# Kernel optimization log

Hardware: AMD Instinct MI355X
Metric: run time of the kernel (lower is better)

## Reference

```python
import jax, jax.numpy as jnp
import numpy as np

B, H, W, C = 2, 96, 192, 768
NH, HD = 12, 64
W0, W1 = 8, 8          # window size
S0, S1 = 4, 4          # shift size
N = W0 * W1
NW = (H // W0) * (W // W1)
HID = 3072             # mlp_ratio 4 * dim
SCALE = HD ** -0.5


def _ln(x, g, b):
    m = x.mean(-1, keepdims=True)
    v = ((x - m) ** 2).mean(-1, keepdims=True)
    return (x - m) * jax.lax.rsqrt(v + 1e-5) * g + b


def _partition(x):  # (B,H,W,C) -> (B*NW, W0, W1, C)
    Bb = x.shape[0]
    x = x.reshape(Bb, H // W0, W0, W // W1, W1, -1).transpose(0, 1, 3, 2, 4, 5)
    return x.reshape(-1, W0, W1, x.shape[-1])


def _reverse(w):  # (B*NW, W0, W1, C) -> (B,H,W,C)
    Cc = w.shape[-1]
    x = w.reshape(B, H // W0, W // W1, W0, W1, Cc).transpose(0, 1, 3, 2, 4, 5)
    return x.reshape(B, H, W, Cc)


def _rope2(x):  # axial 2D RoPE on (nB, W0, W1, HD): first half rotates over h, second over w
    dh = HD // 2

    def cs(L, d):
        inv = 1.0 / (10000.0 ** (jnp.arange(0, d, 2, dtype=jnp.float32) / d))
        ang = jnp.arange(L, dtype=jnp.float32)[:, None] * inv
        return jnp.cos(ang), jnp.sin(ang)

    def rot(xa, cos, sin):
        x1, x2 = xa[..., 0::2], xa[..., 1::2]
        return jnp.stack([x1 * cos - x2 * sin, x1 * sin + x2 * cos], -1).reshape(xa.shape)

    ch, sh = cs(W0, dh)
    cw, sw = cs(W1, dh)
    xh = rot(x[..., :dh], ch[:, None, :], sh[:, None, :])
    xw = rot(x[..., dh:], cw[None, :, :], sw[None, :, :])
    return jnp.concatenate([xh, xw], -1)


def _make_mask():
    # faithful port of BasicLayer.create_mask (2D path)
    img = np.zeros((H, W), np.float32)
    cnt = 0
    for hs in (slice(0, -W0), slice(-W0, -S0), slice(-S0, None)):
        for wsl in (slice(0, -W1), slice(-W1, 0), slice(0, None)):
            img[hs, wsl] = cnt
            cnt += 1
    mw = img.reshape(H // W0, W0, W // W1, W1).transpose(0, 2, 1, 3).reshape(NW, N)
    am = mw[:, None, :] - mw[:, :, None]
    return jnp.asarray(np.where(am != 0, -100.0, 0.0).astype(np.float32))


def setup_inputs():
    key = jax.random.key(0)
    ks = jax.random.split(key, 6)
    s = lambda k, shape, fan: jax.random.normal(k, shape, jnp.float32) * (fan ** -0.5)
    return dict(
        x=jax.random.normal(ks[0], (B, H * W, C), jnp.float32),
        mask=_make_mask(),
        w_qkv=s(ks[1], (3 * C, C), C), b_qkv=jnp.zeros((3 * C,), jnp.float32),
        w_proj=s(ks[2], (C, C), C), b_proj=jnp.zeros((C,), jnp.float32),
        g1=jnp.ones((C,), jnp.float32), b1=jnp.zeros((C,), jnp.float32),
        g2=jnp.ones((C,), jnp.float32), b2=jnp.zeros((C,), jnp.float32),
        w_fc1=s(ks[3], (HID, C), C), b_fc1=jnp.zeros((HID,), jnp.float32),
        w_fc2=s(ks[4], (C, HID), HID), b_fc2=jnp.zeros((C,), jnp.float32),
    )


def reference(x, mask, w_qkv, b_qkv, w_proj, b_proj, g1, b1, g2, b2,
              w_fc1, b_fc1, w_fc2, b_fc2):
    shortcut = x
    xi = x.reshape(B, H, W, C)
    xi = jnp.roll(xi, (-S0, -S1), axis=(1, 2))
    xw = _partition(xi).reshape(-1, N, C)  # (B*NW, N, C)
    B_ = xw.shape[0]
    qkv = (xw @ w_qkv.T + b_qkv).reshape(B_, N, 3, NH, HD).transpose(2, 0, 3, 1, 4)
    q, k, v = qkv[0], qkv[1], qkv[2]  # (B_, NH, N, HD)
    q = _rope2(q.reshape(-1, W0, W1, HD)).reshape(B_, NH, N, HD)
    k = _rope2(k.reshape(-1, W0, W1, HD)).reshape(B_, NH, N, HD)
    attn = jnp.einsum('bhnd,bhmd->bhnm', q * SCALE, k)
    attn = attn.reshape(B, NW, NH, N, N) + mask[None, :, None]
    attn = jax.nn.softmax(attn.reshape(B_, NH, N, N), axis=-1)
    out = jnp.einsum('bhnm,bhmd->bnhd', attn, v).reshape(B_, N, C)
    out = out @ w_proj.T + b_proj
    xr = _reverse(out.reshape(-1, W0, W1, C))
    xr = jnp.roll(xr, (S0, S1), axis=(1, 2)).reshape(B, H * W, C)
    x1 = _ln(shortcut + xr, g1, b1)          # post-norm residual, as in source
    h = jax.nn.relu(x1 @ w_fc1.T + b_fc1) @ w_fc2.T + b_fc2
    return _ln(x1 + h, g2, b2)
```

## Files before the change

### kernel.cpp

```cpp
#include <hip/hip_runtime.h>
#include <math.h>
#include <stddef.h>

#define NTOK   36864
#define CDIM   768
#define HIDDIM 3072
#define QKVDIM 2304

typedef unsigned short u16;
typedef unsigned int   u32;
typedef __attribute__((ext_vector_type(8))) short short8;
typedef __attribute__((ext_vector_type(4))) float f32x4;

__device__ __forceinline__ float bf2f(u16 h) { return __uint_as_float(((u32)h) << 16); }
__device__ __forceinline__ u16 f2bf(float f) {
  u32 u = __float_as_uint(f);
  u32 r = u + 0x7fffu + ((u >> 16) & 1u);
  return (u16)(r >> 16);
}

__device__ __forceinline__ int win_row_to_src(int r) {
  int n = r & 63;
  int wflat = r >> 6;
  int b = wflat / 288;
  int wi = wflat - b * 288;
  int wh = wi / 24;
  int ww = wi - wh * 24;
  int i0 = n >> 3, i1 = n & 7;
  int hh = wh * 8 + i0 + 4; if (hh >= 96)  hh -= 96;
  int wp = ww * 8 + i1 + 4; if (wp >= 192) wp -= 192;
  return b * 18432 + hh * 192 + wp;
}

__device__ __forceinline__ void load_lds16(const u16* g, u16* l) {
  __builtin_amdgcn_global_load_lds((const __attribute__((address_space(1))) void*)g,
                                   (__attribute__((address_space(3))) void*)l, 16, 0, 0);
}

template<int OUTBF, int RELU, int RES>
__launch_bounds__(512, 2)
__global__ void gemm256(const u16* __restrict__ A, const u16* __restrict__ Wt,
                        const float* __restrict__ bias, const u16* __restrict__ res,
                        void* __restrict__ Cout, int M, int N, int K,
                        int gridx, int nwg)
{
  const int orig = blockIdx.x;
  const int xcd  = orig & 7;
  const int q    = nwg >> 3, r8 = nwg & 7;
  const int wgid = (xcd < r8 ? xcd * (q + 1) : r8 * (q + 1) + (xcd - r8) * q) + (orig >> 3);
  const int bn   = (wgid % gridx) * 256;
  const int bm   = (wgid / gridx) * 256;

  __shared__ __align__(16) u16 lds[2][2][256 * 64];

  const int t    = threadIdx.x;
  const int wv   = t >> 6, lane = t & 63;
  const int wm   = wv >> 2, wn = wv & 3;
  const int lr   = lane & 15, lg = lane >> 4;
  const int sr   = t >> 3;
  const int ss   = t & 7;

  const u16* Abase = A  + (size_t)bm * K;
  const u16* Bbase = Wt + (size_t)bn * K;

  const int nt = K >> 6;

  auto stage = [&](int kt, int b) {
    const int k0 = kt << 6;
#pragma unroll
    for (int j = 0; j < 4; j++) {
      int row  = j * 64 + sr;
      int slot = ss ^ (row & 7);
      load_lds16(Abase + (size_t)row * K + k0 + slot * 8, &lds[b][0][j * 4096 + t * 8]);
    }
#pragma unroll
    for (int j = 0; j < 4; j++) {
      int row  = j * 64 + sr;
      int slot = ss ^ (row & 7);
      load_lds16(Bbase + (size_t)row * K + k0 + slot * 8, &lds[b][1][j * 4096 + t * 8]);
    }
  };

  f32x4 acc[8][4] = {};

  stage(0, 0);
  stage(1, 1);

  for (int tt = 0; tt < nt; tt++) {
    const int cur = tt & 1;
    if (tt + 1 < nt) asm volatile("s_waitcnt vmcnt(8)" ::: "memory");
    else             asm volatile("s_waitcnt vmcnt(0)" ::: "memory");
    __builtin_amdgcn_s_barrier();

    const u16* Ab = &lds[cur][0][0];
    const u16* Bb = &lds[cur][1][0];

    short8 bfr[4][2], afr[4][2];
#pragma unroll
    for (int nf = 0; nf < 4; nf++)
#pragma unroll
      for (int ks = 0; ks < 2; ks++) {
        int row = wn * 64 + nf * 16 + lr;
        bfr[nf][ks] = *(const short8*)(Bb + row * 64 + (((ks * 4 + lg) ^ (row & 7)) << 3));
      }
#pragma unroll
    for (int mf = 0; mf < 4; mf++)
#pragma unroll
      for (int ks = 0; ks < 2; ks++) {
        int row = wm * 128 + mf * 16 + lr;
        afr[mf][ks] = *(const short8*)(Ab + row * 64 + (((ks * 4 + lg) ^ (row & 7)) << 3));
      }
    asm volatile("s_waitcnt lgkmcnt(0)" ::: "memory");
    __builtin_amdgcn_sched_barrier(0);
    __builtin_amdgcn_s_setprio(1);
#pragma unroll
    for (int ks = 0; ks < 2; ks++)
#pragma unroll
      for (int mf = 0; mf < 4; mf++)
#pragma unroll
        for (int nf = 0; nf < 4; nf++)
          acc[mf][nf] = __builtin_amdgcn_mfma_f32_16x16x32_bf16(afr[mf][ks], bfr[nf][ks], acc[mf][nf], 0, 0, 0);
    __builtin_amdgcn_s_setprio(0);

    short8 afr2[4][2];
#pragma unroll
    for (int mf = 0; mf < 4; mf++)
#pragma unroll
      for (int ks = 0; ks < 2; ks++) {
        int row = wm * 128 + (mf + 4) * 16 + lr;
        afr2[mf][ks] = *(const short8*)(Ab + row * 64 + (((ks * 4 + lg) ^ (row & 7)) << 3));
      }
    asm volatile("s_waitcnt lgkmcnt(0)" ::: "memory");
    __builtin_amdgcn_sched_barrier(0);
    __builtin_amdgcn_s_barrier();

    if (tt + 2 < nt) stage(tt + 2, cur);

    __builtin_amdgcn_s_setprio(1);
#pragma unroll
    for (int ks = 0; ks < 2; ks++)
#pragma unroll
      for (int mf = 0; mf < 4; mf++)
#pragma unroll
        for (int nf = 0; nf < 4; nf++)
          acc[mf + 4][nf] = __builtin_amdgcn_mfma_f32_16x16x32_bf16(afr2[mf][ks], bfr[nf][ks], acc[mf + 4][nf], 0, 0, 0);
    __builtin_amdgcn_s_setprio(0);
  }

#pragma unroll
  for (int nf = 0; nf < 4; nf++) {
    int col = bn + wn * 64 + nf * 16 + lr;
    float bcol = bias[col];
#pragma unroll
    for (int mf = 0; mf < 8; mf++) {
#pragma unroll
      for (int j = 0; j < 4; j++) {
        int row = bm + wm * 128 + mf * 16 + lg * 4 + j;
        float v = acc[mf][nf][j] + bcol;
        if (RELU) v = fmaxf(v, 0.f);
        if (RES)  v += bf2f(res[(size_t)row * N + col]);
        if (OUTBF) ((u16*)Cout)[(size_t)row * N + col] = f2bf(v);
        else       ((float*)Cout)[(size_t)row * N + col] = v;
      }
    }
  }
}

__launch_bounds__(256)
__global__ void gather_x_bf16(const float* __restrict__ x, u16* __restrict__ xg)
{
  const int r = blockIdx.x, t = threadIdx.x;
  const float* src = x + (size_t)win_row_to_src(r) * CDIM;
  u16* dst = xg + (size_t)r * CDIM;
#pragma unroll
  for (int e = 0; e < 3; e++) dst[t + 256 * e] = f2bf(src[t + 256 * e]);
}

__launch_bounds__(256)
__global__ void conv_bf16(const float* __restrict__ in, u16* __restrict__ out, int n)
{
  int i = blockIdx.x * 256 + threadIdx.x;
  if (i < n) out[i] = f2bf(in[i]);
}

__launch_bounds__(256)
__global__ void attn_mfma(const u16* __restrict__ qkv, const float* __restrict__ mask,
                          u16* __restrict__ out, int bw0)
{
  __shared__ u16 vt[4][4096];
  __shared__ u16 pbuf[4][4096];
  __shared__ float ropetab[512];

  const int t = threadIdx.x;
  {
    int p = t >> 3, pos = t & 7;
    float inv = __expf(-(float)(p & 15) * 0.5756462732485115f);
    float sv, cv;
    sincosf((float)pos * inv, &sv, &cv);
    ropetab[t * 2]     = cv;
    ropetab[t * 2 + 1] = sv;
  }
  __syncthreads();

  const int wv = t >> 6, lane = t & 63;
  const int lr = lane & 15, lg = lane >> 4;
  const int gp   = blockIdx.x * 4 + wv;
  const int head = gp % 12;
  const int lw   = gp / 12;
  const int bwg  = bw0 + lw;
  const int widx = bwg % 288;
  const u16* base = qkv + (size_t)lw * 64 * QKVDIM + head * 64;

  {
    const u16* vrow = base + 1536 + (size_t)lane * QKVDIM;
    u16* vb = vt[wv];
#pragma unroll
    for (int s = 0; s < 8; s++) {
      short8 v = *(const short8*)(vrow + s * 8);
#pragma unroll
      for (int j = 0; j < 8; j++) {
        int d = s * 8 + j;
        vb[d * 64 + ((((lane >> 3) ^ (d & 7)) << 3) | (lane & 7))] = (u16)v[j];
      }
    }
  }

  short8 aq[4][2], ak[4][2];
#pragma unroll
  for (int f = 0; f < 4; f++) {
#pragma unroll
    for (int ks = 0; ks < 2; ks++) {
      int n = f * 16 + lr;
      short8 qv = *(const short8*)(base + (size_t)n * QKVDIM + ks * 32 + lg * 8);
      short8 kv = *(const short8*)(base + (size_t)n * QKVDIM + 768 + ks * 32 + lg * 8);
      short8 qo, ko;
#pragma unroll
      for (int jj = 0; jj < 4; jj++) {
        int p   = ks * 16 + lg * 4 + jj;
        int pos = (p < 16) ? (n >> 3) : (n & 7);
        float cv = ropetab[(p * 8 + pos) * 2];
        float sv = ropetab[(p * 8 + pos) * 2 + 1];
        float q1 = bf2f((u16)qv[2 * jj]), q2 = bf2f((u16)qv[2 * jj + 1]);
        float k1 = bf2f((u16)kv[2 * jj]), k2 = bf2f((u16)kv[2 * jj + 1]);
        qo[2 * jj]     = (short)f2bf((q1 * cv - q2 * sv) * 0.125f);
        qo[2 * jj + 1] = (short)f2bf((q1 * sv + q2 * cv) * 0.125f);
        ko[2 * jj]     = (short)f2bf(k1 * cv - k2 * sv);
        ko[2 * jj + 1] = (short)f2bf(k1 * sv + k2 * cv);
      }
      aq[f][ks] = qo; ak[f][ks] = ko;
    }
  }

  f32x4 sf[4][4] = {};
#pragma unroll
  for (int ks = 0; ks < 2; ks++)
#pragma unroll
    for (int fn = 0; fn < 4; fn++)
#pragma unroll
      for (int fm = 0; fm < 4; fm++)
        sf[fn][fm] = __builtin_amdgcn_mfma_f32_16x16x32_bf16(aq[fn][ks], ak[fm][ks], sf[fn][fm], 0, 0, 0);

  const float* mrow = mask + (size_t)widx * 4096;
#pragma unroll
  for (int fn = 0; fn < 4; fn++)
#pragma unroll
    for (int fm = 0; fm < 4; fm++)
#pragma unroll
      for (int j = 0; j < 4; j++)
        sf[fn][fm][j] += mrow[(fn * 16 + lg * 4 + j) * 64 + fm * 16 + lr];

#pragma unroll
  for (int fn = 0; fn < 4; fn++) {
#pragma unroll
    for (int j = 0; j < 4; j++) {
      float m0 = fmaxf(fmaxf(sf[fn][0][j], sf[fn][1][j]),
                       fmaxf(sf[fn][2][j], sf[fn][3][j]));
      m0 = fmaxf(m0, __shfl_xor(m0, 1));
      m0 = fmaxf(m0, __shfl_xor(m0, 2));
      m0 = fmaxf(m0, __shfl_xor(m0, 4));
      m0 = fmaxf(m0, __shfl_xor(m0, 8));
      float s0 = 0.f;
#pragma unroll
      for (int fm = 0; fm < 4; fm++) {
        float e = __expf(sf[fn][fm][j] - m0);
        sf[fn][fm][j] = e;
        s0 += e;
      }
      s0 += __shfl_xor(s0, 1);
      s0 += __shfl_xor(s0, 2);
      s0 += __shfl_xor(s0, 4);
      s0 += __shfl_xor(s0, 8);
      float r = 1.f / s0;
#pragma unroll
      for (int fm = 0; fm < 4; fm++) sf[fn][fm][j] *= r;
    }
  }

  u16* pb = pbuf[wv];
#pragma unroll
  for (int fn = 0; fn < 4; fn++)
#pragma unroll
    for (int fm = 0; fm < 4; fm++)
#pragma unroll
      for (int j = 0; j < 4; j++) {
        int n = fn * 16 + lg * 4 + j, m = fm * 16 + lr;
        pb[n * 64 + ((((m >> 3) ^ (n & 7)) << 3) | (m & 7))] = f2bf(sf[fn][fm][j]);
      }
  asm volatile("s_waitcnt lgkmcnt(0)" ::: "memory");
  __builtin_amdgcn_sched_barrier(0);

  short8 ap[4][2], bvf[4][2];
#pragma unroll
  for (int f = 0; f < 4; f++)
#pragma unroll
    for (int ks = 0; ks < 2; ks++) {
      int rn = f * 16 + lr;
      ap[f][ks]  = *(const short8*)(pb     + rn * 64 + (((ks * 4 + lg) ^ (rn & 7)) << 3));
      bvf[f][ks] = *(const short8*)(vt[wv] + rn * 64 + (((ks * 4 + lg) ^ (rn & 7)) << 3));
    }
  f32x4 o[4][4] = {};
#pragma unroll
  for (int ks = 0; ks < 2; ks++)
#pragma unroll
    for (int fn = 0; fn < 4; fn++)
#pragma unroll
      for (int fd = 0; fd < 4; fd++)
        o[fn][fd] = __builtin_amdgcn_mfma_f32_16x16x32_bf16(ap[fn][ks], bvf[fd][ks], o[fn][fd], 0, 0, 0);

  u16* ob = out + ((size_t)bwg * 64) * CDIM + head * 64;
#pragma unroll
  for (int fn = 0; fn < 4; fn++)
#pragma unroll
    for (int fd = 0; fd < 4; fd++)
#pragma unroll
      for (int j = 0; j < 4; j++) {
        int n = fn * 16 + lg * 4 + j, d = fd * 16 + lr;
        ob[(size_t)n * CDIM + d] = f2bf(o[fn][fd][j]);
      }
}

__launch_bounds__(256)
__global__ void ln1_kernel(const float* __restrict__ xin, const u16* __restrict__ add,
                           const float* __restrict__ g, const float* __restrict__ bb,
                           u16* __restrict__ out)
{
  const int tok = blockIdx.x;
  int b = tok / 18432;
  int hw = tok - b * 18432;
  int h = hw / 192, w = hw - h * 192;
  int h2 = h - 4; if (h2 < 0) h2 += 96;
  int w2 = w - 4; if (w2 < 0) w2 += 192;
  int r = ((b * 12 + (h2 >> 3)) * 24 + (w2 >> 3)) * 64 + (h2 & 7) * 8 + (w2 & 7);
  const float* a0 = xin + (size_t)tok * CDIM;
  const u16*   a1 = add + (size_t)r * CDIM;

  const int t = threadIdx.x;
  float v[3];
  float s1 = 0.f, s2 = 0.f;
#pragma unroll
  for (int e = 0; e < 3; e++) {
    float x = a0[t + 256 * e] + bf2f(a1[t + 256 * e]);
    v[e] = x; s1 += x; s2 += x * x;
  }
  __shared__ float r1[256], r2[256];
  r1[t] = s1; r2[t] = s2;
  __syncthreads();
  for (int o = 128; o > 0; o >>= 1) {
    if (t < o) { r1[t] += r1[t + o]; r2[t] += r2[t + o]; }
    __syncthreads();
  }
  float mean = r1[0] * (1.f / 768.f);
  float var  = r2[0] * (1.f / 768.f) - mean * mean;
  float rs   = rsqrtf(var + 1e-5f);
#pragma unroll
  for (int e = 0; e < 3; e++) {
    int c = t + 256 * e;
    out[(size_t)tok * CDIM + c] = f2bf((v[e] - mean) * rs * g[c] + bb[c]);
  }
}

__launch_bounds__(256)
__global__ void ln2_kernel(const u16* __restrict__ xin, const float* __restrict__ g,
                           const float* __restrict__ bb, float* __restrict__ out)
{
  const int tok = blockIdx.x;
  const u16* a0 = xin + (size_t)tok * CDIM;
  const int t = threadIdx.x;
  float v[3];
  float s1 = 0.f, s2 = 0.f;
#pragma unroll
  for (int e = 0; e < 3; e++) {
    float x = bf2f(a0[t + 256 * e]);
    v[e] = x; s1 += x; s2 += x * x;
  }
  __shared__ float r1[256], r2[256];
  r1[t] = s1; r2[t] = s2;
  __syncthreads();
  for (int o = 128; o > 0; o >>= 1) {
    if (t < o) { r1[t] += r1[t + o]; r2[t] += r2[t + o]; }
    __syncthreads();
  }
  float mean = r1[0] * (1.f / 768.f);
  float var  = r2[0] * (1.f / 768.f) - mean * mean;
  float rs   = rsqrtf(var + 1e-5f);
#pragma unroll
  for (int e = 0; e < 3; e++) {
    int c = t + 256 * e;
    out[(size_t)tok * CDIM + c] = (v[e] - mean) * rs * g[c] + bb[c];
  }
}

static inline void launch_gemm(const u16* A, const u16* Wt, const float* bias,
                               const u16* res, void* C, int M, int N, int K,
                               int outbf, int relu, int resf, hipStream_t s)
{
  int gridx = N / 256, nwg = gridx * (M / 256);
  if (outbf) {
    if (relu)      gemm256<1,1,0><<<nwg, 512, 0, s>>>(A, Wt, bias, res, C, M, N, K, gridx, nwg);
    else if (resf) gemm256<1,0,1><<<nwg, 512, 0, s>>>(A, Wt, bias, res, C, M, N, K, gridx, nwg);
    else           gemm256<1,0,0><<<nwg, 512, 0, s>>>(A, Wt, bias, res, C, M, N, K, gridx, nwg);
  } else {
    gemm256<0,0,0><<<nwg, 512, 0, s>>>(A, Wt, bias, res, C, M, N, K, gridx, nwg);
  }
}

extern "C" void kernel_launch(void* const* d_in, const int* in_sizes, int n_in,
                              void* d_out, int out_size, void* d_ws, size_t ws_size,
                              hipStream_t stream)
{
  const float* x      = (const float*)d_in[0];
  const float* mask   = (const float*)d_in[1];
  const float* w_qkv  = (const float*)d_in[2];
  const float* b_qkv  = (const float*)d_in[3];
  const float* w_proj = (const float*)d_in[4];
  const float* b_proj = (const float*)d_in[5];
  const float* g1     = (const float*)d_in[6];
  const float* b1     = (const float*)d_in[7];
  const float* g2     = (const float*)d_in[8];
  const float* b2     = (const float*)d_in[9];
  const float* w_fc1  = (const float*)d_in[10];
  const float* b_fc1  = (const float*)d_in[11];
  const float* w_fc2  = (const float*)d_in[12];
  const float* b_fc2  = (const float*)d_in[13];
  float* out = (float*)d_out;

  char* base = (char*)d_ws;
  u16* R1 = (u16*)base;
  u16* R2 = (u16*)(base + 56623104);
  u16* AO = R2 + 28311552;
  u16* R3 = (u16*)(base + 56623104 + 113246208);
  u16* wqkvb  = (u16*)(base + 56623104 + 113246208 + 56623104);
  u16* wprojb = wqkvb  + 1769472;
  u16* wfc1b  = wprojb + 589824;
  u16* wfc2b  = wfc1b  + 2359296;

  conv_bf16<<<(1769472 + 255) / 256, 256, 0, stream>>>(w_qkv,  wqkvb,  1769472);
  conv_bf16<<<( 589824 + 255) / 256, 256, 0, stream>>>(w_proj, wprojb,  589824);
  conv_bf16<<<(2359296 + 255) / 256, 256, 0, stream>>>(w_fc1,  wfc1b,  2359296);
  conv_bf16<<<(2359296 + 255) / 256, 256, 0, stream>>>(w_fc2,  wfc2b,  2359296);
  gather_x_bf16<<<NTOK, 256, 0, stream>>>(x, R1);

  for (int c = 0; c < 3; c++) {
    launch_gemm(R1 + (size_t)c * 12288 * CDIM, wqkvb, b_qkv, nullptr, R2,
                12288, QKVDIM, CDIM, 1, 0, 0, stream);
    attn_mfma<<<576, 256, 0, stream>>>(R2, mask, AO, c * 192);
  }

  launch_gemm(AO, wprojb, b_proj, nullptr, R3, NTOK, CDIM, CDIM, 1, 0, 0, stream);

  ln1_kernel<<<NTOK, 256, 0, stream>>>(x, R3, g1, b1, R1);

  for (int c = 0; c < 2; c++) {
    const u16* x1c = R1 + (size_t)c * 18432 * CDIM;
    launch_gemm(x1c, wfc1b, b_fc1, nullptr, R2, 18432, HIDDIM, CDIM, 1, 1, 0, stream);
    launch_gemm(R2, wfc2b, b_fc2, x1c, R3 + (size_t)c * 18432 * CDIM,
                18432, CDIM, HIDDIM, 1, 0, 1, stream);
  }

  ln2_kernel<<<NTOK, 256, 0, stream>>>(R3, g2, b2, out);
}
```

Measured before the change: 953.8 us.

## Restructure GEMM main loop into 8-phase half-tile ping-pong pipeline

```diff
diff --git a/kernel.cpp b/kernel.cpp
--- a/kernel.cpp
+++ b/kernel.cpp
@@ -37,6 +37,11 @@
                                    (__attribute__((address_space(3))) void*)l, 16, 0, 0);
 }
 
+#define GBAR()  __builtin_amdgcn_s_barrier()
+#define LGKM0() do { asm volatile("s_waitcnt lgkmcnt(0)" ::: "memory"); \
+                     __builtin_amdgcn_sched_barrier(0); } while (0)
+#define VMC4()  asm volatile("s_waitcnt vmcnt(4)" ::: "memory")
+
 template<int OUTBF, int RELU, int RES>
 __launch_bounds__(512, 2)
 __global__ void gemm256(const u16* __restrict__ A, const u16* __restrict__ Wt,
@@ -57,106 +62,118 @@
   const int wv   = t >> 6, lane = t & 63;
   const int wm   = wv >> 2, wn = wv & 3;
   const int lr   = lane & 15, lg = lane >> 4;
-  const int sr   = t >> 3;
-  const int ss   = t & 7;
+  const int rl   = t >> 3;
+  const int sc   = t & 7;
 
   const u16* Abase = A  + (size_t)bm * K;
   const u16* Bbase = Wt + (size_t)bn * K;
 
-  const int nt = K >> 6;
-
-  auto stage = [&](int kt, int b) {
+  const int nt   = K >> 6;
+  const int half = nt >> 1;
+
+  auto stageA = [&](int kt, int mh, int b) {
     const int k0 = kt << 6;
 #pragma unroll
-    for (int j = 0; j < 4; j++) {
-      int row  = j * 64 + sr;
-      int slot = ss ^ (row & 7);
-      load_lds16(Abase + (size_t)row * K + k0 + slot * 8, &lds[b][0][j * 4096 + t * 8]);
-    }
-#pragma unroll
-    for (int j = 0; j < 4; j++) {
-      int row  = j * 64 + sr;
-      int slot = ss ^ (row & 7);
-      load_lds16(Bbase + (size_t)row * K + k0 + slot * 8, &lds[b][1][j * 4096 + t * 8]);
+    for (int j = 0; j < 2; j++) {
+      int row  = j * 128 + mh * 64 + rl;
+      int slot = sc ^ (row & 7);
+      load_lds16(Abase + (size_t)row * K + k0 + slot * 8, &lds[b][0][row * 64 + sc * 8]);
     }
   };
+  auto stageB = [&](int kt, int nh, int b) {
+    const int k0 = kt << 6;
+#pragma unroll
+    for (int j = 0; j < 2; j++) {
+      int row  = j * 128 + nh * 32 + rl + (rl & 32);
+      int slot = sc ^ (row & 7);
+      load_lds16(Bbase + (size_t)row * K + k0 + slot * 8, &lds[b][1][row * 64 + sc * 8]);
+    }
+  };
+
+  short8 af[4][2], bf0[2][2], bf1[2][2];
+  auto lda = [&](const u16* Ab, int mh) {
+#pragma unroll
+    for (int mf = 0; mf < 4; mf++)
+#pragma unroll
+      for (int ks = 0; ks < 2; ks++) {
+        int row = wm * 128 + mh * 64 + mf * 16 + lr;
+        af[mf][ks] = *(const short8*)(Ab + row * 64 + (((ks * 4 + lg) ^ (row & 7)) << 3));
+      }
+  };
+  auto ldb = [&](const u16* Bb, int nh, short8 bf[2][2]) {
+#pragma unroll
+    for (int nf = 0; nf < 2; nf++)
+#pragma unroll
+      for (int ks = 0; ks < 2; ks++) {
+        int row = wn * 64 + nh * 32 + nf * 16 + lr;
+        bf[nf][ks] = *(const short8*)(Bb + row * 64 + (((ks * 4 + lg) ^ (row & 7)) << 3));
+      }
+  };
 
   f32x4 acc[8][4] = {};
-
-  stage(0, 0);
-  stage(1, 1);
-
-  for (int tt = 0; tt < nt; tt++) {
-    const int cur = tt & 1;
-    if (tt + 1 < nt) asm volatile("s_waitcnt vmcnt(8)" ::: "memory");
-    else             asm volatile("s_waitcnt vmcnt(0)" ::: "memory");
-    __builtin_amdgcn_s_barrier();
-
-    const u16* Ab = &lds[cur][0][0];
-    const u16* Bb = &lds[cur][1][0];
-
-    short8 bfr[4][2], afr[4][2];
-#pragma unroll
-    for (int nf = 0; nf < 4; nf++)
-#pragma unroll
-      for (int ks = 0; ks < 2; ks++) {
-        int row = wn * 64 + nf * 16 + lr;
-        bfr[nf][ks] = *(const short8*)(Bb + row * 64 + (((ks * 4 + lg) ^ (row & 7)) << 3));
-      }
-#pragma unroll
-    for (int mf = 0; mf < 4; mf++)
-#pragma unroll
-      for (int ks = 0; ks < 2; ks++) {
-        int row = wm * 128 + mf * 16 + lr;
-        afr[mf][ks] = *(const short8*)(Ab + row * 64 + (((ks * 4 + lg) ^ (row & 7)) << 3));
-      }
-    asm volatile("s_waitcnt lgkmcnt(0)" ::: "memory");
-    __builtin_amdgcn_sched_barrier(0);
+  auto mfma16 = [&](short8 bf[2][2], int mh, int nh) {
     __builtin_amdgcn_s_setprio(1);
 #pragma unroll
     for (int ks = 0; ks < 2; ks++)
 #pragma unroll
       for (int mf = 0; mf < 4; mf++)
 #pragma unroll
-        for (int nf = 0; nf < 4; nf++)
-          acc[mf][nf] = __builtin_amdgcn_mfma_f32_16x16x32_bf16(afr[mf][ks], bfr[nf][ks], acc[mf][nf], 0, 0, 0);
+        for (int nf = 0; nf < 2; nf++)
+          acc[mh * 4 + mf][nh * 2 + nf] =
+            __builtin_amdgcn_mfma_f32_16x16x32_bf16(af[mf][ks], bf[nf][ks],
+                                                    acc[mh * 4 + mf][nh * 2 + nf], 0, 0, 0);
     __builtin_amdgcn_s_setprio(0);
-
-    short8 afr2[4][2];
-#pragma unroll
-    for (int mf = 0; mf < 4; mf++)
-#pragma unroll
-      for (int ks = 0; ks < 2; ks++) {
-        int row = wm * 128 + (mf + 4) * 16 + lr;
-        afr2[mf][ks] = *(const short8*)(Ab + row * 64 + (((ks * 4 + lg) ^ (row & 7)) << 3));
-      }
-    asm volatile("s_waitcnt lgkmcnt(0)" ::: "memory");
-    __builtin_amdgcn_sched_barrier(0);
-    __builtin_amdgcn_s_barrier();
-
-    if (tt + 2 < nt) stage(tt + 2, cur);
-
-    __builtin_amdgcn_s_setprio(1);
-#pragma unroll
-    for (int ks = 0; ks < 2; ks++)
-#pragma unroll
-      for (int mf = 0; mf < 4; mf++)
-#pragma unroll
-        for (int nf = 0; nf < 4; nf++)
-          acc[mf + 4][nf] = __builtin_amdgcn_mfma_f32_16x16x32_bf16(afr2[mf][ks], bfr[nf][ks], acc[mf + 4][nf], 0, 0, 0);
-    __builtin_amdgcn_s_setprio(0);
-  }
-
-#pragma unroll
-  for (int nf = 0; nf < 4; nf++) {
-    int col = bn + wn * 64 + nf * 16 + lr;
+  };
+
+  stageA(0, 0, 0); stageB(0, 0, 0); stageA(0, 1, 0); stageB(0, 1, 0);
+  stageA(1, 0, 1); stageB(1, 0, 1);
+  VMC4();
+  GBAR();
+
+  const u16* A0 = &lds[0][0][0]; const u16* B0 = &lds[0][1][0];
+  const u16* A1 = &lds[1][0][0]; const u16* B1 = &lds[1][1][0];
+
+  for (int i = 0; i < half; i++) {
+    const int kt1 = 2 * i + 1;
+    const bool more = (i + 1 < half);
+    lda(A0, 0); ldb(B0, 0, bf0);
+    stageA(kt1, 1, 1);
+    GBAR(); LGKM0(); mfma16(bf0, 0, 0); GBAR();
+    ldb(B0, 1, bf1);
+    stageB(kt1, 1, 1);
+    GBAR(); LGKM0(); mfma16(bf1, 0, 1); GBAR();
+    lda(A0, 1);
+    if (more) stageA(kt1 + 1, 0, 0);
+    GBAR(); LGKM0(); mfma16(bf0, 1, 0); GBAR();
+    if (more) stageB(kt1 + 1, 0, 0);
+    GBAR(); LGKM0(); mfma16(bf1, 1, 1);
+    VMC4();
+    GBAR();
+    lda(A1, 0); ldb(B1, 0, bf0);
+    if (more) stageA(kt1 + 1, 1, 0);
+    GBAR(); LGKM0(); mfma16(bf0, 0, 0); GBAR();
+    ldb(B1, 1, bf1);
+    if (more) stageB(kt1 + 1, 1, 0);
+    GBAR(); LGKM0(); mfma16(bf1, 0, 1); GBAR();
+    lda(A1, 1);
+    if (more) stageA(kt1 + 2, 0, 1);
+    GBAR(); LGKM0(); mfma16(bf0, 1, 0); GBAR();
+    if (more) stageB(kt1 + 2, 0, 1);
+    GBAR(); LGKM0(); mfma16(bf1, 1, 1);
+    VMC4();
+    GBAR();
+  }
+
+#pragma unroll
+  for (int b = 0; b < 4; b++) {
+    int col = bn + wn * 64 + (b >> 1) * 32 + (b & 1) * 16 + lr;
     float bcol = bias[col];
 #pragma unroll
-    for (int mf = 0; mf < 8; mf++) {
+    for (int a = 0; a < 8; a++) {
 #pragma unroll
       for (int j = 0; j < 4; j++) {
-        int row = bm + wm * 128 + mf * 16 + lg * 4 + j;
-        float v = acc[mf][nf][j] + bcol;
+        int row = bm + wm * 128 + (a >> 2) * 64 + (a & 3) * 16 + lg * 4 + j;
+        float v = acc[a][b][j] + bcol;
         if (RELU) v = fmaxf(v, 0.f);
         if (RES)  v += bf2f(res[(size_t)row * N + col]);
         if (OUTBF) ((u16*)Cout)[(size_t)row * N + col] = f2bf(v);
```

Result: slower. 1.438 ms (+50.8%).

## Interleave LDS fragment loads with MFMA groups and move the barrier to the loop tail

Applied to the files above, without the earlier changes.

```diff
diff --git a/kernel.cpp b/kernel.cpp
--- a/kernel.cpp
+++ b/kernel.cpp
@@ -37,6 +37,8 @@
                                    (__attribute__((address_space(3))) void*)l, 16, 0, 0);
 }
 
+#define SB() __builtin_amdgcn_sched_barrier(0)
+
 template<int OUTBF, int RELU, int RES>
 __launch_bounds__(512, 2)
 __global__ void gemm256(const u16* __restrict__ A, const u16* __restrict__ Wt,
@@ -85,66 +87,92 @@
 
   stage(0, 0);
   stage(1, 1);
+  asm volatile("s_waitcnt vmcnt(8)" ::: "memory");
+  __builtin_amdgcn_s_barrier();
 
   for (int tt = 0; tt < nt; tt++) {
     const int cur = tt & 1;
-    if (tt + 1 < nt) asm volatile("s_waitcnt vmcnt(8)" ::: "memory");
-    else             asm volatile("s_waitcnt vmcnt(0)" ::: "memory");
-    __builtin_amdgcn_s_barrier();
-
     const u16* Ab = &lds[cur][0][0];
     const u16* Bb = &lds[cur][1][0];
 
-    short8 bfr[4][2], afr[4][2];
-#pragma unroll
-    for (int nf = 0; nf < 4; nf++)
-#pragma unroll
-      for (int ks = 0; ks < 2; ks++) {
-        int row = wn * 64 + nf * 16 + lr;
-        bfr[nf][ks] = *(const short8*)(Bb + row * 64 + (((ks * 4 + lg) ^ (row & 7)) << 3));
-      }
+    short8 b0[4], b1[4], a00[4], a10[4], a01[4], a11[4];
+#pragma unroll
+    for (int nf = 0; nf < 4; nf++) {
+      int row = wn * 64 + nf * 16 + lr;
+      b0[nf] = *(const short8*)(Bb + row * 64 + ((lg ^ (row & 7)) << 3));
+    }
+#pragma unroll
+    for (int mf = 0; mf < 4; mf++) {
+      int row = wm * 128 + mf * 16 + lr;
+      a00[mf] = *(const short8*)(Ab + row * 64 + ((lg ^ (row & 7)) << 3));
+    }
+    SB();
+#pragma unroll
+    for (int mf = 0; mf < 4; mf++) {
+      int row = wm * 128 + 64 + mf * 16 + lr;
+      a10[mf] = *(const short8*)(Ab + row * 64 + ((lg ^ (row & 7)) << 3));
+    }
+#pragma unroll
+    for (int nf = 0; nf < 4; nf++) {
+      int row = wn * 64 + nf * 16 + lr;
+      b1[nf] = *(const short8*)(Bb + row * 64 + (((4 + lg) ^ (row & 7)) << 3));
+    }
+    SB();
+    asm volatile("s_waitcnt lgkmcnt(8)" ::: "memory"); SB();
+#pragma unroll
+    for (int mf = 0; mf < 4; mf++) {
+      int row = wm * 128 + mf * 16 + lr;
+      a01[mf] = *(const short8*)(Ab + row * 64 + (((4 + lg) ^ (row & 7)) << 3));
+    }
+    SB();
+    __builtin_amdgcn_s_setprio(1);
 #pragma unroll
     for (int mf = 0; mf < 4; mf++)
 #pragma unroll
-      for (int ks = 0; ks < 2; ks++) {
-        int row = wm * 128 + mf * 16 + lr;
-        afr[mf][ks] = *(const short8*)(Ab + row * 64 + (((ks * 4 + lg) ^ (row & 7)) << 3));
-      }
-    asm volatile("s_waitcnt lgkmcnt(0)" ::: "memory");
-    __builtin_amdgcn_sched_barrier(0);
+      for (int nf = 0; nf < 4; nf++)
+        acc[mf][nf] = __builtin_amdgcn_mfma_f32_16x16x32_bf16(a00[mf], b0[nf], acc[mf][nf], 0, 0, 0);
+    __builtin_amdgcn_s_setprio(0);
+#pragma unroll
+    for (int mf = 0; mf < 4; mf++) {
+      int row = wm * 128 + 64 + mf * 16 + lr;
+      a11[mf] = *(const short8*)(Ab + row * 64 + (((4 + lg) ^ (row & 7)) << 3));
+    }
+    SB();
+    asm volatile("s_waitcnt lgkmcnt(8)" ::: "memory"); SB();
     __builtin_amdgcn_s_setprio(1);
 #pragma unroll
-    for (int ks = 0; ks < 2; ks++)
-#pragma unroll
-      for (int mf = 0; mf < 4; mf++)
-#pragma unroll
-        for (int nf = 0; nf < 4; nf++)
-          acc[mf][nf] = __builtin_amdgcn_mfma_f32_16x16x32_bf16(afr[mf][ks], bfr[nf][ks], acc[mf][nf], 0, 0, 0);
+    for (int mf = 0; mf < 4; mf++)
+#pragma unroll
+      for (int nf = 0; nf < 4; nf++)
+        acc[4 + mf][nf] = __builtin_amdgcn_mfma_f32_16x16x32_bf16(a10[mf], b0[nf], acc[4 + mf][nf], 0, 0, 0);
     __builtin_amdgcn_s_setprio(0);
-
-    short8 afr2[4][2];
+    asm volatile("s_waitcnt lgkmcnt(4)" ::: "memory"); SB();
+    __builtin_amdgcn_s_setprio(1);
 #pragma unroll
     for (int mf = 0; mf < 4; mf++)
 #pragma unroll
-      for (int ks = 0; ks < 2; ks++) {
-        int row = wm * 128 + (mf + 4) * 16 + lr;
-        afr2[mf][ks] = *(const short8*)(Ab + row * 64 + (((ks * 4 + lg) ^ (row & 7)) << 3));
-      }
-    asm volatile("s_waitcnt lgkmcnt(0)" ::: "memory");
-    __builtin_amdgcn_sched_barrier(0);
+      for (int nf = 0; nf < 4; nf++)
+        acc[mf][nf] = __builtin_amdgcn_mfma_f32_16x16x32_bf16(a01[mf], b1[nf], acc[mf][nf], 0, 0, 0);
+    __builtin_amdgcn_s_setprio(0);
+    asm volatile("s_waitcnt lgkmcnt(0)" ::: "memory"); SB();
+    __builtin_amdgcn_s_setprio(1);
+#pragma unroll
+    for (int mf = 0; mf < 4; mf++)
+#pragma unroll
+      for (int nf = 0; nf < 4; nf++)
+        acc[4 + mf][nf] = __builtin_amdgcn_mfma_f32_16x16x32_bf16(a11[mf], b1[nf], acc[4 + mf][nf], 0, 0, 0);
+    __builtin_amdgcn_s_setprio(0);
+
     __builtin_amdgcn_s_barrier();
-
-    if (tt + 2 < nt) stage(tt + 2, cur);
-
-    __builtin_amdgcn_s_setprio(1);
-#pragma unroll
-    for (int ks = 0; ks < 2; ks++)
-#pragma unroll
-      for (int mf = 0; mf < 4; mf++)
-#pragma unroll
-        for (int nf = 0; nf < 4; nf++)
-          acc[mf + 4][nf] = __builtin_amdgcn_mfma_f32_16x16x32_bf16(afr2[mf][ks], bfr[nf][ks], acc[mf + 4][nf], 0, 0, 0);
-    __builtin_amdgcn_s_setprio(0);
+    if (tt + 1 < nt) {
+      if (tt + 2 < nt) {
+        stage(tt + 2, cur);
+        asm volatile("s_waitcnt vmcnt(8)" ::: "memory");
+      } else {
+        asm volatile("s_waitcnt vmcnt(0)" ::: "memory");
+      }
+      __builtin_amdgcn_s_barrier();
+    }
   }
 
 #pragma unroll
```

New measurement: 0.9997 ms. 4.8% more time.
